# Kernel optimization log

Hardware: AMD Instinct MI355X
Metric: run time of the kernel (lower is better)

## Reference

```python
import jax, jax.numpy as jnp
import numpy as np

N = 50000   # nodes
E = 800000  # edges
F = 64      # num_node_features
H = 64      # hidden_channels
NB = 3      # num_blocks
G = 64      # graphs in batch
C = 10      # num_classes
EPS = 1e-5  # BatchNorm eps


def setup_inputs() -> dict:
    key = jax.random.key(0)
    ks = jax.random.split(key, 24)
    x = jax.random.normal(ks[0], (N, F), dtype=jnp.float32)
    edge_index = jax.random.randint(ks[1], (2, E), 0, N, dtype=jnp.int64)
    batch = jnp.sort(jax.random.randint(ks[2], (N,), 0, G, dtype=jnp.int64))
    s = 0.05
    inp = {
        "x": x, "edge_index": edge_index, "batch": batch,
        "pre_w": jax.random.normal(ks[3], (F, H)) * s,
        "pre_b": jnp.zeros((H,), jnp.float32),
        # stacked per-block params (blocks are structurally identical)
        "blk_prelu1": jnp.full((NB,), 0.25, jnp.float32),
        "blk_bn_gamma": jnp.ones((NB, H), jnp.float32),
        "blk_bn_beta": jnp.zeros((NB, H), jnp.float32),
        "blk_w1": jax.random.normal(ks[4], (NB, H, 2 * H)) * s,
        "blk_b1": jnp.zeros((NB, 2 * H), jnp.float32),
        "blk_prelu2": jnp.full((NB,), 0.25, jnp.float32),
        "blk_w2": jax.random.normal(ks[5], (NB, 2 * H, H)) * s,
        "blk_b2": jnp.zeros((NB, H), jnp.float32),
        "post_bn_gamma": jnp.ones((H,), jnp.float32),
        "post_bn_beta": jnp.zeros((H,), jnp.float32),
        "fc1_w": jax.random.normal(ks[6], (H, 4 * H)) * s,
        "fc1_b": jnp.zeros((4 * H,), jnp.float32),
        "post_prelu": jnp.asarray(0.25, jnp.float32),
        "fc2_w": jax.random.normal(ks[7], (4 * H, C)) * s,
        "fc2_b": jnp.zeros((C,), jnp.float32),
    }
    return inp


def _prelu(x, a):
    return jnp.where(x >= 0, x, a * x)


def _batchnorm(x, gamma, beta):
    # training-mode BN over the node dimension (biased variance), as in torch
    mean = jnp.mean(x, axis=0)
    var = jnp.var(x, axis=0)
    return (x - mean) * jax.lax.rsqrt(var + EPS) * gamma + beta


def _gcn_conv(x, W, bias, src, dst):
    # PyG GCNConv: linear transform, then D^-1/2 (A+I) D^-1/2 aggregation, then bias.
    h = x @ W                                   # [N, out]
    deg = jax.ops.segment_sum(jnp.ones((E,), h.dtype), dst, num_segments=N) + 1.0
    dinv = jax.lax.rsqrt(deg)                   # [N]
    norm = dinv[src] * dinv[dst]                # [E]
    agg = jax.ops.segment_sum(h[src] * norm[:, None], dst, num_segments=N)
    agg = agg + h * (dinv * dinv)[:, None]      # self-loop contribution
    return agg + bias


def reference(x, edge_index, batch, pre_w, pre_b,
              blk_prelu1, blk_bn_gamma, blk_bn_beta, blk_w1, blk_b1,
              blk_prelu2, blk_w2, blk_b2,
              post_bn_gamma, post_bn_beta, fc1_w, fc1_b, post_prelu, fc2_w, fc2_b):
    src, dst = edge_index[0], edge_index[1]
    h = x @ pre_w + pre_b                       # [N, H]
    for i in range(NB):
        h = _prelu(h, blk_prelu1[i])
        h = _batchnorm(h, blk_bn_gamma[i], blk_bn_beta[i])
        h = _gcn_conv(h, blk_w1[i], blk_b1[i], src, dst)   # [N, 2H]
        h = _prelu(h, blk_prelu2[i])
        h = _gcn_conv(h, blk_w2[i], blk_b2[i], src, dst)   # [N, H]
    # global mean pool per graph
    sums = jax.ops.segment_sum(h, batch, num_segments=G)   # [G, H]
    cnts = jax.ops.segment_sum(jnp.ones((N,), h.dtype), batch, num_segments=G)
    pooled = sums / jnp.maximum(cnts, 1.0)[:, None]
    out = _batchnorm(pooled, post_bn_gamma, post_bn_beta)
    out = out @ fc1_w + fc1_b
    out = _prelu(out, post_prelu)
    # dropout with p=0.0 is identity
    out = out @ fc2_w + fc2_b                   # [G, C]
    return out
```

## Files before the change

kernel.cpp:

```cpp
#include <hip/hip_runtime.h>
#include <hip/hip_fp16.h>

#define NN 50000
#define NE 800000
#define NG 64
#define NC 10
#define BN_EPS 1e-5f
#define NSB 196

typedef __attribute__((ext_vector_type(2))) _Float16 h2v;
typedef __attribute__((ext_vector_type(8))) _Float16 f16x8;
typedef __attribute__((ext_vector_type(4))) float f32x4;

__device__ __forceinline__ float2 up2(unsigned u) {
    __half2 h = *reinterpret_cast<__half2*>(&u);
    return __half22float2(h);
}
__device__ __forceinline__ unsigned pk2(float a, float b) {
    __half2 h = __floats2half2_rn(a, b);
    return *reinterpret_cast<unsigned*>(&h);
}
__device__ __forceinline__ float fdot2u(unsigned a, unsigned b, float c) {
    return __builtin_amdgcn_fdot2(__builtin_bit_cast(h2v, a), __builtin_bit_cast(h2v, b), c, false);
}


__global__ void deg_count_kernel(const int* __restrict__ dst, int* __restrict__ deg,
                                 unsigned short* __restrict__ pos16) {
    int e = blockIdx.x * blockDim.x + threadIdx.x;
    if (e < NE) {
        int d = __builtin_nontemporal_load(&dst[e]);
        unsigned short p = (unsigned short)atomicAdd(&deg[d], 1);
        __builtin_nontemporal_store(p, &pos16[e]);
    }
}

__global__ __launch_bounds__(256) void block_sum_kernel(const int* __restrict__ deg,
                                                        int* __restrict__ bsum) {
    int b = blockIdx.x, t = threadIdx.x;
    int n = b * 256 + t;
    int v = (n < NN) ? deg[n] : 0;
    __shared__ int red[256];
    red[t] = v;
    __syncthreads();
    for (int off = 128; off > 0; off >>= 1) {
        if (t < off) red[t] += red[t + off];
        __syncthreads();
    }
    if (t == 0) bsum[b] = red[0];
}

__global__ __launch_bounds__(256) void bsum_scan_kernel(const int* __restrict__ bsum,
                                                        int* __restrict__ boff) {
    __shared__ int s[256];
    int t = threadIdx.x;
    int v = (t < NSB) ? bsum[t] : 0;
    s[t] = v;
    __syncthreads();
    for (int off = 1; off < 256; off <<= 1) {
        int cur = s[t];
        int add = (t >= off) ? s[t - off] : 0;
        __syncthreads();
        s[t] = cur + add;
        __syncthreads();
    }
    if (t < NSB) boff[t] = s[t] - v;
}

__global__ __launch_bounds__(256) void csr_setup_kernel(const int* __restrict__ deg,
                                                        const int* __restrict__ boff,
                                                        int* __restrict__ row_off,
                                                        float* __restrict__ dinv,
                                                        float* __restrict__ rdeg) {
    int b = blockIdx.x, t = threadIdx.x;
    int n = b * 256 + t;
    int v = (n < NN) ? deg[n] : 0;
    __shared__ int s[256];
    s[t] = v;
    __syncthreads();
    for (int off = 1; off < 256; off <<= 1) {
        int cur = s[t];
        int add = (t >= off) ? s[t - off] : 0;
        __syncthreads();
        s[t] = cur + add;
        __syncthreads();
    }
    int excl = s[t] - v + boff[b];
    if (n < NN) {
        row_off[n] = excl;
        float d = (float)v + 1.0f;
        dinv[n] = rsqrtf(d);
        rdeg[n] = sqrtf(d);
    }
    if (n == NN - 1) row_off[NN] = NE;
}

__global__ void scatter_csr_kernel(const int* __restrict__ src, const int* __restrict__ dst,
                                   const unsigned short* __restrict__ pos16,
                                   const int* __restrict__ row_off,
                                   int* __restrict__ csr_src) {
    int e = blockIdx.x * blockDim.x + threadIdx.x;
    if (e >= NE) return;
    int s = __builtin_nontemporal_load(&src[e]);
    int d = __builtin_nontemporal_load(&dst[e]);
    int p = (int)__builtin_nontemporal_load(&pos16[e]);
    csr_src[row_off[d] + p] = s;
}

__global__ void arow_kernel(const int* __restrict__ row_off, const int* __restrict__ csr_src,
                            const float* __restrict__ dinv, float* __restrict__ arow) {
    int n = blockIdx.x * 256 + threadIdx.x;
    if (n >= NN) return;
    float dv = dinv[n];
    float s = dv;
    int e0 = row_off[n], e1 = row_off[n + 1];
    for (int i = e0; i < e1; ++i) s += dinv[csr_src[i]];
    arow[n] = dv * s;
}


__global__ __launch_bounds__(256) void bn_stats_kernel(const __half* __restrict__ h,
                                                       const float* __restrict__ rdeg,
                                                       const float* __restrict__ alpha_p,
                                                       float* __restrict__ stats) {
    float alpha = alpha_p[0];
    int tid = threadIdx.x;
    int c4 = (tid & 15) * 4;
    int rg = tid >> 4;
    float sx = 0, sy = 0, sz = 0, sw = 0;
    float qx = 0, qy = 0, qz = 0, qw = 0;
    for (int n = blockIdx.x * 16 + rg; n < NN; n += gridDim.x * 16) {
        float rd = rdeg[n];
        uint2 u = *(const uint2*)&h[(size_t)n * 64 + c4];
        float2 lo = up2(u.x), hi = up2(u.y);
        float a = lo.x >= 0.f ? lo.x : alpha * lo.x;
        float b = lo.y >= 0.f ? lo.y : alpha * lo.y;
        float c = hi.x >= 0.f ? hi.x : alpha * hi.x;
        float d = hi.y >= 0.f ? hi.y : alpha * hi.y;
        a *= rd; b *= rd; c *= rd; d *= rd;
        sx += a; sy += b; sz += c; sw += d;
        qx += a * a; qy += b * b; qz += c * c; qw += d * d;
    }
    __shared__ float ls[256 * 8];
    float* p = &ls[tid * 8];
    p[0] = sx; p[1] = sy; p[2] = sz; p[3] = sw;
    p[4] = qx; p[5] = qy; p[6] = qz; p[7] = qw;
    __syncthreads();
    if (tid < 128) {
        int cidx = tid >> 3;
        int j = tid & 7;
        float acc = 0.f;
        for (int r = 0; r < 16; ++r) acc += ls[(r * 16 + cidx) * 8 + j];
        int ch = cidx * 4 + (j & 3);
        if (j < 4) atomicAdd(&stats[ch], acc);
        else       atomicAdd(&stats[64 + ch], acc);
    }
}


template <bool PRELU, int OUT>
__global__ __launch_bounds__(256) void gather_kernel(const int* __restrict__ row_off,
                                                     const int* __restrict__ csr_src,
                                                     const float* __restrict__ dinv,
                                                     const float* __restrict__ bias,
                                                     const float* __restrict__ alpha_p,
                                                     const __half* __restrict__ hh,
                                                     __half* __restrict__ outp) {
    int tid = threadIdx.x;
    int r = blockIdx.x * 32 + (tid >> 3);
    int c = blockIdx.y * 32 + (tid & 7) * 4;
    if (r >= NN) return;
    float alpha = 0.f;
    if constexpr (PRELU) alpha = alpha_p[0];
    uint2 u0 = *(const uint2*)&hh[(size_t)r * 64 + c];
    float2 slo = up2(u0.x), shi = up2(u0.y);
    float ax = slo.x, ay = slo.y, az = shi.x, aw = shi.y;
    if constexpr (PRELU) {
        ax = ax >= 0.f ? ax : alpha * ax;
        ay = ay >= 0.f ? ay : alpha * ay;
        az = az >= 0.f ? az : alpha * az;
        aw = aw >= 0.f ? aw : alpha * aw;
    }
    int beg = row_off[r];
    int end = row_off[r + 1];
    int i = beg;
    for (; i + 3 < end; i += 4) {
        int s0 = csr_src[i], s1 = csr_src[i + 1], s2 = csr_src[i + 2], s3 = csr_src[i + 3];
        uint2 v0 = *(const uint2*)&hh[(size_t)s0 * 64 + c];
        uint2 v1 = *(const uint2*)&hh[(size_t)s1 * 64 + c];
        uint2 v2 = *(const uint2*)&hh[(size_t)s2 * 64 + c];
        uint2 v3 = *(const uint2*)&hh[(size_t)s3 * 64 + c];
        float2 a0 = up2(v0.x), b0 = up2(v0.y);
        float2 a1 = up2(v1.x), b1 = up2(v1.y);
        float2 a2 = up2(v2.x), b2 = up2(v2.y);
        float2 a3 = up2(v3.x), b3 = up2(v3.y);
        if constexpr (PRELU) {
            a0.x = a0.x >= 0.f ? a0.x : alpha * a0.x;  a0.y = a0.y >= 0.f ? a0.y : alpha * a0.y;
            b0.x = b0.x >= 0.f ? b0.x : alpha * b0.x;  b0.y = b0.y >= 0.f ? b0.y : alpha * b0.y;
            a1.x = a1.x >= 0.f ? a1.x : alpha * a1.x;  a1.y = a1.y >= 0.f ? a1.y : alpha * a1.y;
            b1.x = b1.x >= 0.f ? b1.x : alpha * b1.x;  b1.y = b1.y >= 0.f ? b1.y : alpha * b1.y;
            a2.x = a2.x >= 0.f ? a2.x : alpha * a2.x;  a2.y = a2.y >= 0.f ? a2.y : alpha * a2.y;
            b2.x = b2.x >= 0.f ? b2.x : alpha * b2.x;  b2.y = b2.y >= 0.f ? b2.y : alpha * b2.y;
            a3.x = a3.x >= 0.f ? a3.x : alpha * a3.x;  a3.y = a3.y >= 0.f ? a3.y : alpha * a3.y;
            b3.x = b3.x >= 0.f ? b3.x : alpha * b3.x;  b3.y = b3.y >= 0.f ? b3.y : alpha * b3.y;
        }
        ax += (a0.x + a1.x) + (a2.x + a3.x);
        ay += (a0.y + a1.y) + (a2.y + a3.y);
        az += (b0.x + b1.x) + (b2.x + b3.x);
        aw += (b0.y + b1.y) + (b2.y + b3.y);
    }
    for (; i < end; ++i) {
        int s0 = csr_src[i];
        uint2 v0 = *(const uint2*)&hh[(size_t)s0 * 64 + c];
        float2 a0 = up2(v0.x), b0 = up2(v0.y);
        if constexpr (PRELU) {
            a0.x = a0.x >= 0.f ? a0.x : alpha * a0.x;  a0.y = a0.y >= 0.f ? a0.y : alpha * a0.y;
            b0.x = b0.x >= 0.f ? b0.x : alpha * b0.x;  b0.y = b0.y >= 0.f ? b0.y : alpha * b0.y;
        }
        ax += a0.x; ay += a0.y; az += b0.x; aw += b0.y;
    }
    float dv = dinv[r];
    float ox, oy, oz, ow;
    if constexpr (OUT == 2) {
        ox = dv * ax; oy = dv * ay; oz = dv * az; ow = dv * aw;
    } else {
        float4 b = *(const float4*)&bias[c];
        ox = dv * ax + b.x; oy = dv * ay + b.y; oz = dv * az + b.z; ow = dv * aw + b.w;
        if constexpr (OUT == 1) {
            ox *= dv; oy *= dv; oz *= dv; ow *= dv;
        }
    }
    uint2 o;
    o.x = pk2(ox, oy);
    o.y = pk2(oz, ow);
    *(uint2*)&outp[(size_t)r * 64 + c] = o;
}


__global__ __launch_bounds__(256) void gemm_pre_kernel(const float* __restrict__ Af,
                                                       const float* __restrict__ W,
                                                       __half* __restrict__ outp,
                                                       const float* __restrict__ bias,
                                                       const float* __restrict__ dinv) {
    constexpr int K = 64, M = 64, BM = 128;
    constexpr int CG = M / 8;
    constexpr int RG = 256 / CG;
    constexpr int KP = K / 2;
    __shared__ unsigned Wh[KP * M];
    __shared__ unsigned Ahs[BM][KP + 4];
    int tid = threadIdx.x;
    for (int i = tid; i < KP * M; i += 256) {
        int kp = i / M, j = i % M;
        Wh[i] = pk2(W[(2 * kp) * M + j], W[(2 * kp + 1) * M + j]);
    }
    int r0 = blockIdx.x * BM;
    for (int i = tid; i < BM * (K / 4); i += 256) {
        int row = i / (K / 4);
        int k4 = (i % (K / 4)) * 4;
        int rr = r0 + row;
        if (rr > NN - 1) rr = NN - 1;
        float4 v = *(const float4*)&Af[(size_t)rr * K + k4];
        uint2 o;
        o.x = pk2(v.x, v.y);
        o.y = pk2(v.z, v.w);
        *(uint2*)&Ahs[row][k4 >> 1] = o;
    }
    __syncthreads();
    int cg = tid % CG, rg = tid / CG;
    int c = cg * 8;
    float acc[4][8];
#pragma unroll
    for (int r = 0; r < 4; ++r)
#pragma unroll
        for (int j = 0; j < 8; ++j) acc[r][j] = 0.f;
#pragma unroll 4
    for (int kp = 0; kp < KP; kp += 2) {
        uint2 a2[4];
#pragma unroll
        for (int r = 0; r < 4; ++r) a2[r] = *(const uint2*)&Ahs[rg + r * RG][kp];
#pragma unroll
        for (int kk = 0; kk < 2; ++kk) {
            const unsigned* wp = &Wh[(kp + kk) * M + c];
            uint4 w0 = *(const uint4*)wp;
            uint4 w1 = *(const uint4*)(wp + 4);
#pragma unroll
            for (int r = 0; r < 4; ++r) {
                unsigned av = kk ? a2[r].y : a2[r].x;
                acc[r][0] = fdot2u(av, w0.x, acc[r][0]);
                acc[r][1] = fdot2u(av, w0.y, acc[r][1]);
                acc[r][2] = fdot2u(av, w0.z, acc[r][2]);
                acc[r][3] = fdot2u(av, w0.w, acc[r][3]);
                acc[r][4] = fdot2u(av, w1.x, acc[r][4]);
                acc[r][5] = fdot2u(av, w1.y, acc[r][5]);
                acc[r][6] = fdot2u(av, w1.z, acc[r][6]);
                acc[r][7] = fdot2u(av, w1.w, acc[r][7]);
            }
        }
    }
    float4 b0 = *(const float4*)&bias[c];
    float4 b1 = *(const float4*)&bias[c + 4];
#pragma unroll
    for (int r = 0; r < 4; ++r) {
        int row = r0 + rg + r * RG;
        if (row < NN) {
            float sc = dinv[row];
            uint4 o;
            o.x = pk2((acc[r][0] + b0.x) * sc, (acc[r][1] + b0.y) * sc);
            o.y = pk2((acc[r][2] + b0.z) * sc, (acc[r][3] + b0.w) * sc);
            o.z = pk2((acc[r][4] + b1.x) * sc, (acc[r][5] + b1.y) * sc);
            o.w = pk2((acc[r][6] + b1.z) * sc, (acc[r][7] + b1.w) * sc);
            *(uint4*)&outp[(size_t)row * M + c] = o;
        }
    }
}


__global__ __launch_bounds__(256) void mfma_gemm1_kernel(const __half* __restrict__ t,
                                                         const float* __restrict__ W1,
                                                         const float* __restrict__ b1,
                                                         __half* __restrict__ u,
                                                         const float* __restrict__ stats,
                                                         const float* __restrict__ gamma,
                                                         const float* __restrict__ beta,
                                                         const float* __restrict__ arow) {
    __shared__ _Float16 At[128][72];
    __shared__ _Float16 Wt[128][72];
    __shared__ float scS[64], shS[64];
    int tid = threadIdx.x;
    if (tid < 64) {
        float mean = stats[tid] * (1.0f / NN);
        float var  = stats[64 + tid] * (1.0f / NN) - mean * mean;
        float sc = gamma[tid] * rsqrtf(var + BN_EPS);
        scS[tid] = sc;
        shS[tid] = beta[tid] - mean * sc;
    }
    for (int i = tid; i < 128 * 32; i += 256) {
        int j = i & 127;
        int k2 = i >> 7;
        *(unsigned*)&Wt[j][2 * k2] = pk2(W1[(2 * k2) * 128 + j], W1[(2 * k2 + 1) * 128 + j]);
    }
    __syncthreads();
    int r0 = blockIdx.x * 128;
    for (int i = tid; i < 128 * 16; i += 256) {
        int row = i >> 4;
        int k4 = (i & 15) * 4;
        int rr = r0 + row;
        if (rr > NN - 1) rr = NN - 1;
        uint2 uu = *(const uint2*)&t[(size_t)rr * 64 + k4];
        float2 lo = up2(uu.x), hi = up2(uu.y);
        float av = arow[rr];
        float vx = lo.x * scS[k4 + 0] + shS[k4 + 0] * av;
        float vy = lo.y * scS[k4 + 1] + shS[k4 + 1] * av;
        float vz = hi.x * scS[k4 + 2] + shS[k4 + 2] * av;
        float vw = hi.y * scS[k4 + 3] + shS[k4 + 3] * av;
        *(unsigned*)&At[row][k4]     = pk2(vx, vy);
        *(unsigned*)&At[row][k4 + 2] = pk2(vz, vw);
    }
    __syncthreads();
    int w = tid >> 6;
    int l = tid & 63;
    int lr = l & 15;
    int lk = (l >> 4) * 8;
    f32x4 acc[2][8];
#pragma unroll
    for (int rt = 0; rt < 2; ++rt)
#pragma unroll
        for (int ct = 0; ct < 8; ++ct) acc[rt][ct] = (f32x4){0.f, 0.f, 0.f, 0.f};
#pragma unroll
    for (int k0 = 0; k0 < 64; k0 += 32) {
        f16x8 a0 = *(const f16x8*)&At[w * 32 + lr][k0 + lk];
        f16x8 a1 = *(const f16x8*)&At[w * 32 + 16 + lr][k0 + lk];
#pragma unroll
        for (int ct = 0; ct < 8; ++ct) {
            f16x8 b = *(const f16x8*)&Wt[ct * 16 + lr][k0 + lk];
            acc[0][ct] = __builtin_amdgcn_mfma_f32_16x16x32_f16(a0, b, acc[0][ct], 0, 0, 0);
            acc[1][ct] = __builtin_amdgcn_mfma_f32_16x16x32_f16(a1, b, acc[1][ct], 0, 0, 0);
        }
    }
    int rowbase = r0 + w * 32 + (l >> 4) * 4;
#pragma unroll
    for (int rt = 0; rt < 2; ++rt) {
#pragma unroll
        for (int ct = 0; ct < 8; ++ct) {
            int col = ct * 16 + lr;
            float bb = b1[col];
#pragma unroll
            for (int r = 0; r < 4; ++r) {
                int row = rowbase + rt * 16 + r;
                if (row < NN) u[(size_t)row * 128 + col] = __float2half(acc[rt][ct][r] + bb);
            }
        }
    }
}


__global__ __launch_bounds__(256) void mfma_gemm2_kernel(const __half* __restrict__ u,
                                                         const float* __restrict__ W2,
                                                         const float* __restrict__ alpha_p,
                                                         const float* __restrict__ dinv,
                                                         __half* __restrict__ t) {
    __shared__ _Float16 Ut[64][136];
    __shared__ _Float16 Wt[64][136];
    int tid = threadIdx.x;
    float alpha = alpha_p[0];
    for (int i = tid; i < 64 * 64; i += 256) {
        int j = i & 63;
        int k2 = i >> 6;
        *(unsigned*)&Wt[j][2 * k2] = pk2(W2[(2 * k2) * 64 + j], W2[(2 * k2 + 1) * 64 + j]);
    }
    int r0 = blockIdx.x * 64;
    for (int i = tid; i < 64 * 32; i += 256) {
        int row = i >> 5;
        int k4 = (i & 31) * 4;
        int rr = r0 + row;
        if (rr > NN - 1) rr = NN - 1;
        uint2 uu = *(const uint2*)&u[(size_t)rr * 128 + k4];
        float2 lo = up2(uu.x), hi = up2(uu.y);
        float vx = lo.x >= 0.f ? lo.x : alpha * lo.x;
        float vy = lo.y >= 0.f ? lo.y : alpha * lo.y;
        float vz = hi.x >= 0.f ? hi.x : alpha * hi.x;
        float vw = hi.y >= 0.f ? hi.y : alpha * hi.y;
        *(unsigned*)&Ut[row][k4]     = pk2(vx, vy);
        *(unsigned*)&Ut[row][k4 + 2] = pk2(vz, vw);
    }
    __syncthreads();
    int w = tid >> 6;
    int l = tid & 63;
    int lr = l & 15;
    int lk = (l >> 4) * 8;
    f32x4 acc[4];
#pragma unroll
    for (int ct = 0; ct < 4; ++ct) acc[ct] = (f32x4){0.f, 0.f, 0.f, 0.f};
#pragma unroll
    for (int k0 = 0; k0 < 128; k0 += 32) {
        f16x8 a = *(const f16x8*)&Ut[w * 16 + lr][k0 + lk];
#pragma unroll
        for (int ct = 0; ct < 4; ++ct) {
            f16x8 b = *(const f16x8*)&Wt[ct * 16 + lr][k0 + lk];
            acc[ct] = __builtin_amdgcn_mfma_f32_16x16x32_f16(a, b, acc[ct], 0, 0, 0);
        }
    }
    int rowbase = r0 + w * 16 + (l >> 4) * 4;
#pragma unroll
    for (int ct = 0; ct < 4; ++ct) {
        int col = ct * 16 + lr;
#pragma unroll
        for (int r = 0; r < 4; ++r) {
            int row = rowbase + r;
            if (row < NN) t[(size_t)row * 64 + col] = __float2half(acc[ct][r] * dinv[row]);
        }
    }
}


__global__ __launch_bounds__(256) void pool_seg_kernel(const __half* __restrict__ h,
                                                       const int* __restrict__ batch,
                                                       float* __restrict__ pooled) {
    int g = blockIdx.x;
    __shared__ int sbeg, send;
    int tid = threadIdx.x;
    if (tid == 0) {
        int lo = 0, hi = NN;
        while (lo < hi) { int mid = (lo + hi) >> 1; if (batch[mid] < g) lo = mid + 1; else hi = mid; }
        sbeg = lo;
        lo = 0; hi = NN;
        while (lo < hi) { int mid = (lo + hi) >> 1; if (batch[mid] < g + 1) lo = mid + 1; else hi = mid; }
        send = lo;
    }
    __syncthreads();
    int beg = sbeg, end = send;
    int c4 = (tid & 15) * 4;
    int rg = tid >> 4;
    float sx = 0, sy = 0, sz = 0, sw = 0;
    for (int n = beg + rg; n < end; n += 16) {
        uint2 u = *(const uint2*)&h[(size_t)n * 64 + c4];
        float2 lo = up2(u.x), hi = up2(u.y);
        sx += lo.x; sy += lo.y; sz += hi.x; sw += hi.y;
    }
    __shared__ float red[256 * 4];
    float* p = &red[tid * 4];
    p[0] = sx; p[1] = sy; p[2] = sz; p[3] = sw;
    __syncthreads();
    if (tid < 64) {
        int cg = tid >> 2;
        int j = tid & 3;
        float acc = 0.f;
        for (int r = 0; r < 16; ++r) acc += red[(r * 16 + cg) * 4 + j];
        float cnt = fmaxf((float)(end - beg), 1.0f);
        pooled[g * 64 + cg * 4 + j] = acc / cnt;
    }
}


__global__ __launch_bounds__(64) void head_stats_kernel(const float* __restrict__ pooled,
                                                        const float* __restrict__ gamma,
                                                        const float* __restrict__ beta,
                                                        float* __restrict__ headsc) {
    int ch = threadIdx.x;
    float s = 0.f, q = 0.f;
    for (int g = 0; g < 64; ++g) {
        float v = pooled[g * 64 + ch];
        s += v; q += v * v;
    }
    float mean = s * (1.0f / 64.0f);
    float var = q * (1.0f / 64.0f) - mean * mean;
    float sc = gamma[ch] * rsqrtf(var + BN_EPS);
    headsc[ch] = sc;
    headsc[64 + ch] = beta[ch] - mean * sc;
}

__global__ __launch_bounds__(256) void head_fc_kernel(const float* __restrict__ pooled,
                                                      const float* __restrict__ headsc,
                                                      const float* __restrict__ fc1w,
                                                      const float* __restrict__ fc1b,
                                                      const float* __restrict__ prelu_p,
                                                      const float* __restrict__ fc2w,
                                                      const float* __restrict__ fc2b,
                                                      float* __restrict__ out) {
    int g = blockIdx.x;
    int tid = threadIdx.x;
    __shared__ float pr[64];
    __shared__ float red[256];
    if (tid < 64) pr[tid] = pooled[g * 64 + tid] * headsc[tid] + headsc[64 + tid];
    __syncthreads();
    float alpha = prelu_p[0];
    float o1 = fc1b[tid];
    for (int k = 0; k < 64; ++k) o1 += pr[k] * fc1w[k * 256 + tid];
    o1 = o1 >= 0.f ? o1 : alpha * o1;
    for (int c = 0; c < NC; ++c) {
        red[tid] = o1 * fc2w[tid * NC + c];
        __syncthreads();
        for (int off = 128; off > 0; off >>= 1) {
            if (tid < off) red[tid] += red[tid + off];
            __syncthreads();
        }
        if (tid == 0) out[g * NC + c] = red[0] + fc2b[c];
        __syncthreads();
    }
}


extern "C" void kernel_launch(void* const* d_in, const int* in_sizes, int n_in,
                              void* d_out, int out_size, void* d_ws, size_t ws_size,
                              hipStream_t stream) {
    const float* x       = (const float*)d_in[0];
    const int*   ei      = (const int*)d_in[1];
    const int*   batch   = (const int*)d_in[2];
    const float* pre_w   = (const float*)d_in[3];
    const float* pre_b   = (const float*)d_in[4];
    const float* bp1     = (const float*)d_in[5];
    const float* bng     = (const float*)d_in[6];
    const float* bnb     = (const float*)d_in[7];
    const float* bw1     = (const float*)d_in[8];
    const float* bb1     = (const float*)d_in[9];
    const float* bp2     = (const float*)d_in[10];
    const float* bw2     = (const float*)d_in[11];
    const float* bb2     = (const float*)d_in[12];
    const float* pgamma  = (const float*)d_in[13];
    const float* pbeta   = (const float*)d_in[14];
    const float* fc1w    = (const float*)d_in[15];
    const float* fc1b    = (const float*)d_in[16];
    const float* pprelu  = (const float*)d_in[17];
    const float* fc2w    = (const float*)d_in[18];
    const float* fc2b    = (const float*)d_in[19];

    const int* src = ei;
    const int* dst = ei + NE;

    __half* hA16 = (__half*)d_ws;
    __half* t16  = hA16 + (size_t)NN * 64;
    __half* u16  = t16 + (size_t)NN * 64;
    float* dinv  = (float*)(u16 + (size_t)NN * 128);
    float* rdeg  = dinv + NN;
    float* arow  = rdeg + NN;
    float* stats = arow + NN;
    float* pooledg = stats + 3 * 128;
    float* headsc  = pooledg + 64 * 64;
    int*   csr_src = (int*)(headsc + 128);
    int*   row_off = csr_src + NE;
    int*   deg     = row_off + NN + 1;
    int*   bsum    = deg + NN;
    int*   boff    = bsum + NSB;
    unsigned short* pos16 = (unsigned short*)(boff + NSB);

    hipMemsetAsync(stats, 0, (size_t)3 * 128 * 4, stream);
    hipMemsetAsync(deg, 0, (size_t)NN * 4, stream);

    deg_count_kernel<<<(NE + 255) / 256, 256, 0, stream>>>(dst, deg, pos16);
    block_sum_kernel<<<NSB, 256, 0, stream>>>(deg, bsum);
    bsum_scan_kernel<<<1, 256, 0, stream>>>(bsum, boff);
    csr_setup_kernel<<<NSB, 256, 0, stream>>>(deg, boff, row_off, dinv, rdeg);
    scatter_csr_kernel<<<(NE + 255) / 256, 256, 0, stream>>>(src, dst, pos16, row_off, csr_src);
    arow_kernel<<<(NN + 255) / 256, 256, 0, stream>>>(row_off, csr_src, dinv, arow);

    gemm_pre_kernel<<<(NN + 127) / 128, 256, 0, stream>>>(x, pre_w, hA16, pre_b, dinv);

    dim3 ggrid((NN + 31) / 32, 2);
    for (int i = 0; i < 3; ++i) {
        const float* a1 = bp1 + i;
        const float* a2 = bp2 + i;
        const float* gm = bng + i * 64;
        const float* bt = bnb + i * 64;
        const float* w1 = bw1 + (size_t)i * 64 * 128;
        const float* b1 = bb1 + i * 128;
        const float* w2 = bw2 + (size_t)i * 128 * 64;
        const float* b2 = bb2 + i * 64;
        float* st = stats + i * 128;

        bn_stats_kernel<<<256, 256, 0, stream>>>(hA16, rdeg, a1, st);
        gather_kernel<true, 2><<<ggrid, 256, 0, stream>>>(
            row_off, csr_src, dinv, nullptr, a1, hA16, t16);
        mfma_gemm1_kernel<<<(NN + 127) / 128, 256, 0, stream>>>(
            t16, w1, b1, u16, st, gm, bt, arow);
        mfma_gemm2_kernel<<<(NN + 63) / 64, 256, 0, stream>>>(
            u16, w2, a2, dinv, t16);
        if (i < 2) {
            gather_kernel<false, 1><<<ggrid, 256, 0, stream>>>(
                row_off, csr_src, dinv, b2, nullptr, t16, hA16);
        } else {
            gather_kernel<false, 0><<<ggrid, 256, 0, stream>>>(
                row_off, csr_src, dinv, b2, nullptr, t16, hA16);
        }
    }

    pool_seg_kernel<<<NG, 256, 0, stream>>>(hA16, batch, pooledg);
    head_stats_kernel<<<1, 64, 0, stream>>>(pooledg, pgamma, pbeta, headsc);
    head_fc_kernel<<<NG, 256, 0, stream>>>(pooledg, headsc, fc1w, fc1b, pprelu,
                                           fc2w, fc2b, (float*)d_out);
}
```

Baseline: 402.5 us.

## Fuse BN stats into gather, merge the two MLP GEMMs, partition CSR scatter

Per-channel BatchNorm statistics are now computed inside the first gather kernel from the self-row load, which removes the separate stats pass. The two MFMA GEMMs are fused into one kernel that keeps the 128-wide intermediate (with PReLU applied) in shared memory instead of writing and re-reading it from global memory. The CSR scatter is split into four passes by destination range, meant to improve write locality at the cost of reading the edge list four times. The fused GEMM uses 64-row tiles and a larger shared footprint, which may lower occupancy.

```diff
diff --git a/kernel.cpp b/kernel.cpp
--- a/kernel.cpp
+++ b/kernel.cpp
@@ -95,14 +95,15 @@
     if (n == NN - 1) row_off[NN] = NE;
 }
 
-__global__ void scatter_csr_kernel(const int* __restrict__ src, const int* __restrict__ dst,
-                                   const unsigned short* __restrict__ pos16,
-                                   const int* __restrict__ row_off,
-                                   int* __restrict__ csr_src) {
+__global__ void scatter_pass_kernel(const int* __restrict__ src, const int* __restrict__ dst,
+                                    const unsigned short* __restrict__ pos16,
+                                    const int* __restrict__ row_off,
+                                    int* __restrict__ csr_src, int d0, int d1) {
     int e = blockIdx.x * blockDim.x + threadIdx.x;
     if (e >= NE) return;
+    int d = __builtin_nontemporal_load(&dst[e]);
+    if (d < d0 || d >= d1) return;
     int s = __builtin_nontemporal_load(&src[e]);
-    int d = __builtin_nontemporal_load(&dst[e]);
     int p = (int)__builtin_nontemporal_load(&pos16[e]);
     csr_src[row_off[d] + p] = s;
 }
@@ -119,77 +120,63 @@
 }
 
 
-__global__ __launch_bounds__(256) void bn_stats_kernel(const __half* __restrict__ h,
-                                                       const float* __restrict__ rdeg,
-                                                       const float* __restrict__ alpha_p,
-                                                       float* __restrict__ stats) {
-    float alpha = alpha_p[0];
-    int tid = threadIdx.x;
-    int c4 = (tid & 15) * 4;
-    int rg = tid >> 4;
-    float sx = 0, sy = 0, sz = 0, sw = 0;
-    float qx = 0, qy = 0, qz = 0, qw = 0;
-    for (int n = blockIdx.x * 16 + rg; n < NN; n += gridDim.x * 16) {
-        float rd = rdeg[n];
-        uint2 u = *(const uint2*)&h[(size_t)n * 64 + c4];
-        float2 lo = up2(u.x), hi = up2(u.y);
-        float a = lo.x >= 0.f ? lo.x : alpha * lo.x;
-        float b = lo.y >= 0.f ? lo.y : alpha * lo.y;
-        float c = hi.x >= 0.f ? hi.x : alpha * hi.x;
-        float d = hi.y >= 0.f ? hi.y : alpha * hi.y;
-        a *= rd; b *= rd; c *= rd; d *= rd;
-        sx += a; sy += b; sz += c; sw += d;
-        qx += a * a; qy += b * b; qz += c * c; qw += d * d;
-    }
-    __shared__ float ls[256 * 8];
-    float* p = &ls[tid * 8];
-    p[0] = sx; p[1] = sy; p[2] = sz; p[3] = sw;
-    p[4] = qx; p[5] = qy; p[6] = qz; p[7] = qw;
-    __syncthreads();
-    if (tid < 128) {
-        int cidx = tid >> 3;
-        int j = tid & 7;
-        float acc = 0.f;
-        for (int r = 0; r < 16; ++r) acc += ls[(r * 16 + cidx) * 8 + j];
-        int ch = cidx * 4 + (j & 3);
-        if (j < 4) atomicAdd(&stats[ch], acc);
-        else       atomicAdd(&stats[64 + ch], acc);
-    }
-}
-
-
-template <bool PRELU, int OUT>
+template <bool PRELU, int OUT, bool STATS>
 __global__ __launch_bounds__(256) void gather_kernel(const int* __restrict__ row_off,
                                                      const int* __restrict__ csr_src,
                                                      const float* __restrict__ dinv,
+                                                     const float* __restrict__ rdeg,
                                                      const float* __restrict__ bias,
                                                      const float* __restrict__ alpha_p,
                                                      const __half* __restrict__ hh,
-                                                     __half* __restrict__ outp) {
+                                                     __half* __restrict__ outp,
+                                                     float* __restrict__ stats) {
     int tid = threadIdx.x;
     int r = blockIdx.x * 32 + (tid >> 3);
     int c = blockIdx.y * 32 + (tid & 7) * 4;
-    if (r >= NN) return;
+    bool valid = r < NN;
+    if constexpr (!STATS) {
+        if (!valid) return;
+    }
+    int rc = valid ? r : NN - 1;
     float alpha = 0.f;
     if constexpr (PRELU) alpha = alpha_p[0];
-    uint2 u0 = *(const uint2*)&hh[(size_t)r * 64 + c];
+    uint2 u0 = *(const uint2*)&hh[(size_t)rc * 64 + c];
     float2 slo = up2(u0.x), shi = up2(u0.y);
-    float ax = slo.x, ay = slo.y, az = shi.x, aw = shi.y;
+    float s0 = slo.x, s1 = slo.y, s2 = shi.x, s3 = shi.y;
     if constexpr (PRELU) {
-        ax = ax >= 0.f ? ax : alpha * ax;
-        ay = ay >= 0.f ? ay : alpha * ay;
-        az = az >= 0.f ? az : alpha * az;
-        aw = aw >= 0.f ? aw : alpha * aw;
-    }
+        s0 = s0 >= 0.f ? s0 : alpha * s0;
+        s1 = s1 >= 0.f ? s1 : alpha * s1;
+        s2 = s2 >= 0.f ? s2 : alpha * s2;
+        s3 = s3 >= 0.f ? s3 : alpha * s3;
+    }
+    if constexpr (STATS) {
+        __shared__ float st[256][8];
+        float rd = valid ? rdeg[rc] : 0.f;
+        float m0 = s0 * rd, m1 = s1 * rd, m2 = s2 * rd, m3 = s3 * rd;
+        float* p = st[tid];
+        p[0] = m0; p[1] = m1; p[2] = m2; p[3] = m3;
+        p[4] = m0 * m0; p[5] = m1 * m1; p[6] = m2 * m2; p[7] = m3 * m3;
+        __syncthreads();
+        if (tid < 64) {
+            int lane8 = tid & 7;
+            int j = tid >> 3;
+            float acc = 0.f;
+            for (int row = 0; row < 32; ++row) acc += st[row * 8 + lane8][j];
+            int ch = blockIdx.y * 32 + lane8 * 4 + (j & 3);
+            atomicAdd(&stats[(j < 4 ? 0 : 64) + ch], acc);
+        }
+        if (!valid) return;
+    }
+    float ax = s0, ay = s1, az = s2, aw = s3;
     int beg = row_off[r];
     int end = row_off[r + 1];
     int i = beg;
     for (; i + 3 < end; i += 4) {
-        int s0 = csr_src[i], s1 = csr_src[i + 1], s2 = csr_src[i + 2], s3 = csr_src[i + 3];
-        uint2 v0 = *(const uint2*)&hh[(size_t)s0 * 64 + c];
-        uint2 v1 = *(const uint2*)&hh[(size_t)s1 * 64 + c];
-        uint2 v2 = *(const uint2*)&hh[(size_t)s2 * 64 + c];
-        uint2 v3 = *(const uint2*)&hh[(size_t)s3 * 64 + c];
+        int q0 = csr_src[i], q1 = csr_src[i + 1], q2 = csr_src[i + 2], q3 = csr_src[i + 3];
+        uint2 v0 = *(const uint2*)&hh[(size_t)q0 * 64 + c];
+        uint2 v1 = *(const uint2*)&hh[(size_t)q1 * 64 + c];
+        uint2 v2 = *(const uint2*)&hh[(size_t)q2 * 64 + c];
+        uint2 v3 = *(const uint2*)&hh[(size_t)q3 * 64 + c];
         float2 a0 = up2(v0.x), b0 = up2(v0.y);
         float2 a1 = up2(v1.x), b1 = up2(v1.y);
         float2 a2 = up2(v2.x), b2 = up2(v2.y);
@@ -210,8 +197,8 @@
         aw += (b0.y + b1.y) + (b2.y + b3.y);
     }
     for (; i < end; ++i) {
-        int s0 = csr_src[i];
-        uint2 v0 = *(const uint2*)&hh[(size_t)s0 * 64 + c];
+        int q0 = csr_src[i];
+        uint2 v0 = *(const uint2*)&hh[(size_t)q0 * 64 + c];
         float2 a0 = up2(v0.x), b0 = up2(v0.y);
         if constexpr (PRELU) {
             a0.x = a0.x >= 0.f ? a0.x : alpha * a0.x;  a0.y = a0.y >= 0.f ? a0.y : alpha * a0.y;
@@ -315,16 +302,21 @@
 }
 
 
-__global__ __launch_bounds__(256) void mfma_gemm1_kernel(const __half* __restrict__ t,
-                                                         const float* __restrict__ W1,
-                                                         const float* __restrict__ b1,
-                                                         __half* __restrict__ u,
-                                                         const float* __restrict__ stats,
-                                                         const float* __restrict__ gamma,
-                                                         const float* __restrict__ beta,
-                                                         const float* __restrict__ arow) {
-    __shared__ _Float16 At[128][72];
-    __shared__ _Float16 Wt[128][72];
+__global__ __launch_bounds__(256) void mfma_mlp_kernel(__half* __restrict__ t,
+                                                       const float* __restrict__ W1,
+                                                       const float* __restrict__ b1,
+                                                       const float* __restrict__ W2,
+                                                       const float* __restrict__ alpha2_p,
+                                                       const float* __restrict__ stats,
+                                                       const float* __restrict__ gamma,
+                                                       const float* __restrict__ beta,
+                                                       const float* __restrict__ arow,
+                                                       const float* __restrict__ dinv) {
+    __shared__ __align__(16) char smem[45056];
+    auto Wt1 = (_Float16(*)[72])smem;
+    auto Wt2 = (_Float16(*)[136])smem;
+    auto At  = (_Float16(*)[72])(smem + 18432);
+    auto Ut  = (_Float16(*)[136])(smem + 27648);
     __shared__ float scS[64], shS[64];
     int tid = threadIdx.x;
     if (tid < 64) {
@@ -337,11 +329,10 @@
     for (int i = tid; i < 128 * 32; i += 256) {
         int j = i & 127;
         int k2 = i >> 7;
-        *(unsigned*)&Wt[j][2 * k2] = pk2(W1[(2 * k2) * 128 + j], W1[(2 * k2 + 1) * 128 + j]);
-    }
-    __syncthreads();
-    int r0 = blockIdx.x * 128;
-    for (int i = tid; i < 128 * 16; i += 256) {
+        *(unsigned*)&Wt1[j][2 * k2] = pk2(W1[(2 * k2) * 128 + j], W1[(2 * k2 + 1) * 128 + j]);
+    }
+    int r0 = blockIdx.x * 64;
+    for (int i = tid; i < 64 * 16; i += 256) {
         int row = i >> 4;
         int k4 = (i & 15) * 4;
         int rr = r0 + row;
@@ -361,93 +352,61 @@
     int l = tid & 63;
     int lr = l & 15;
     int lk = (l >> 4) * 8;
-    f32x4 acc[2][8];
-#pragma unroll
-    for (int rt = 0; rt < 2; ++rt)
-#pragma unroll
-        for (int ct = 0; ct < 8; ++ct) acc[rt][ct] = (f32x4){0.f, 0.f, 0.f, 0.f};
-#pragma unroll
-    for (int k0 = 0; k0 < 64; k0 += 32) {
-        f16x8 a0 = *(const f16x8*)&At[w * 32 + lr][k0 + lk];
-        f16x8 a1 = *(const f16x8*)&At[w * 32 + 16 + lr][k0 + lk];
-#pragma unroll
-        for (int ct = 0; ct < 8; ++ct) {
-            f16x8 b = *(const f16x8*)&Wt[ct * 16 + lr][k0 + lk];
-            acc[0][ct] = __builtin_amdgcn_mfma_f32_16x16x32_f16(a0, b, acc[0][ct], 0, 0, 0);
-            acc[1][ct] = __builtin_amdgcn_mfma_f32_16x16x32_f16(a1, b, acc[1][ct], 0, 0, 0);
-        }
-    }
-    int rowbase = r0 + w * 32 + (l >> 4) * 4;
-#pragma unroll
-    for (int rt = 0; rt < 2; ++rt) {
+    int rloc = w * 16 + (l >> 4) * 4;
+    {
+        f32x4 acc[8];
+#pragma unroll
+        for (int ct = 0; ct < 8; ++ct) acc[ct] = (f32x4){0.f, 0.f, 0.f, 0.f};
+#pragma unroll
+        for (int k0 = 0; k0 < 64; k0 += 32) {
+            f16x8 a = *(const f16x8*)&At[w * 16 + lr][k0 + lk];
+#pragma unroll
+            for (int ct = 0; ct < 8; ++ct) {
+                f16x8 b = *(const f16x8*)&Wt1[ct * 16 + lr][k0 + lk];
+                acc[ct] = __builtin_amdgcn_mfma_f32_16x16x32_f16(a, b, acc[ct], 0, 0, 0);
+            }
+        }
+        float alpha = alpha2_p[0];
 #pragma unroll
         for (int ct = 0; ct < 8; ++ct) {
             int col = ct * 16 + lr;
             float bb = b1[col];
 #pragma unroll
             for (int r = 0; r < 4; ++r) {
-                int row = rowbase + rt * 16 + r;
-                if (row < NN) u[(size_t)row * 128 + col] = __float2half(acc[rt][ct][r] + bb);
+                float v = acc[ct][r] + bb;
+                v = v >= 0.f ? v : alpha * v;
+                Ut[rloc + r][col] = (_Float16)v;
             }
         }
     }
-}
-
-
-__global__ __launch_bounds__(256) void mfma_gemm2_kernel(const __half* __restrict__ u,
-                                                         const float* __restrict__ W2,
-                                                         const float* __restrict__ alpha_p,
-                                                         const float* __restrict__ dinv,
-                                                         __half* __restrict__ t) {
-    __shared__ _Float16 Ut[64][136];
-    __shared__ _Float16 Wt[64][136];
-    int tid = threadIdx.x;
-    float alpha = alpha_p[0];
+    __syncthreads();
     for (int i = tid; i < 64 * 64; i += 256) {
         int j = i & 63;
         int k2 = i >> 6;
-        *(unsigned*)&Wt[j][2 * k2] = pk2(W2[(2 * k2) * 64 + j], W2[(2 * k2 + 1) * 64 + j]);
-    }
-    int r0 = blockIdx.x * 64;
-    for (int i = tid; i < 64 * 32; i += 256) {
-        int row = i >> 5;
-        int k4 = (i & 31) * 4;
-        int rr = r0 + row;
-        if (rr > NN - 1) rr = NN - 1;
-        uint2 uu = *(const uint2*)&u[(size_t)rr * 128 + k4];
-        float2 lo = up2(uu.x), hi = up2(uu.y);
-        float vx = lo.x >= 0.f ? lo.x : alpha * lo.x;
-        float vy = lo.y >= 0.f ? lo.y : alpha * lo.y;
-        float vz = hi.x >= 0.f ? hi.x : alpha * hi.x;
-        float vw = hi.y >= 0.f ? hi.y : alpha * hi.y;
-        *(unsigned*)&Ut[row][k4]     = pk2(vx, vy);
-        *(unsigned*)&Ut[row][k4 + 2] = pk2(vz, vw);
-    }
-    __syncthreads();
-    int w = tid >> 6;
-    int l = tid & 63;
-    int lr = l & 15;
-    int lk = (l >> 4) * 8;
-    f32x4 acc[4];
-#pragma unroll
-    for (int ct = 0; ct < 4; ++ct) acc[ct] = (f32x4){0.f, 0.f, 0.f, 0.f};
-#pragma unroll
-    for (int k0 = 0; k0 < 128; k0 += 32) {
-        f16x8 a = *(const f16x8*)&Ut[w * 16 + lr][k0 + lk];
+        *(unsigned*)&Wt2[j][2 * k2] = pk2(W2[(2 * k2) * 64 + j], W2[(2 * k2 + 1) * 64 + j]);
+    }
+    __syncthreads();
+    {
+        f32x4 acc[4];
+#pragma unroll
+        for (int ct = 0; ct < 4; ++ct) acc[ct] = (f32x4){0.f, 0.f, 0.f, 0.f};
+#pragma unroll
+        for (int k0 = 0; k0 < 128; k0 += 32) {
+            f16x8 a = *(const f16x8*)&Ut[w * 16 + lr][k0 + lk];
+#pragma unroll
+            for (int ct = 0; ct < 4; ++ct) {
+                f16x8 b = *(const f16x8*)&Wt2[ct * 16 + lr][k0 + lk];
+                acc[ct] = __builtin_amdgcn_mfma_f32_16x16x32_f16(a, b, acc[ct], 0, 0, 0);
+            }
+        }
 #pragma unroll
         for (int ct = 0; ct < 4; ++ct) {
-            f16x8 b = *(const f16x8*)&Wt[ct * 16 + lr][k0 + lk];
-            acc[ct] = __builtin_amdgcn_mfma_f32_16x16x32_f16(a, b, acc[ct], 0, 0, 0);
-        }
-    }
-    int rowbase = r0 + w * 16 + (l >> 4) * 4;
-#pragma unroll
-    for (int ct = 0; ct < 4; ++ct) {
-        int col = ct * 16 + lr;
-#pragma unroll
-        for (int r = 0; r < 4; ++r) {
-            int row = rowbase + r;
-            if (row < NN) t[(size_t)row * 64 + col] = __float2half(acc[ct][r] * dinv[row]);
+            int col = ct * 16 + lr;
+#pragma unroll
+            for (int r = 0; r < 4; ++r) {
+                int row = r0 + rloc + r;
+                if (row < NN) t[(size_t)row * 64 + col] = __float2half(acc[ct][r] * dinv[row]);
+            }
         }
     }
 }
@@ -569,8 +528,7 @@
 
     __half* hA16 = (__half*)d_ws;
     __half* t16  = hA16 + (size_t)NN * 64;
-    __half* u16  = t16 + (size_t)NN * 64;
-    float* dinv  = (float*)(u16 + (size_t)NN * 128);
+    float* dinv  = (float*)(t16 + (size_t)NN * 64);
     float* rdeg  = dinv + NN;
     float* arow  = rdeg + NN;
     float* stats = arow + NN;
@@ -590,7 +548,12 @@
     block_sum_kernel<<<NSB, 256, 0, stream>>>(deg, bsum);
     bsum_scan_kernel<<<1, 256, 0, stream>>>(bsum, boff);
     csr_setup_kernel<<<NSB, 256, 0, stream>>>(deg, boff, row_off, dinv, rdeg);
-    scatter_csr_kernel<<<(NE + 255) / 256, 256, 0, stream>>>(src, dst, pos16, row_off, csr_src);
+    for (int p = 0; p < 4; ++p) {
+        int d0 = p * 12500;
+        int d1 = (p == 3) ? NN : d0 + 12500;
+        scatter_pass_kernel<<<(NE + 255) / 256, 256, 0, stream>>>(
+            src, dst, pos16, row_off, csr_src, d0, d1);
+    }
     arow_kernel<<<(NN + 255) / 256, 256, 0, stream>>>(row_off, csr_src, dinv, arow);
 
     gemm_pre_kernel<<<(NN + 127) / 128, 256, 0, stream>>>(x, pre_w, hA16, pre_b, dinv);
@@ -607,19 +570,16 @@
         const float* b2 = bb2 + i * 64;
         float* st = stats + i * 128;
 
-        bn_stats_kernel<<<256, 256, 0, stream>>>(hA16, rdeg, a1, st);
-        gather_kernel<true, 2><<<ggrid, 256, 0, stream>>>(
-            row_off, csr_src, dinv, nullptr, a1, hA16, t16);
-        mfma_gemm1_kernel<<<(NN + 127) / 128, 256, 0, stream>>>(
-            t16, w1, b1, u16, st, gm, bt, arow);
-        mfma_gemm2_kernel<<<(NN + 63) / 64, 256, 0, stream>>>(
-            u16, w2, a2, dinv, t16);
+        gather_kernel<true, 2, true><<<ggrid, 256, 0, stream>>>(
+            row_off, csr_src, dinv, rdeg, nullptr, a1, hA16, t16, st);
+        mfma_mlp_kernel<<<(NN + 63) / 64, 256, 0, stream>>>(
+            t16, w1, b1, w2, a2, st, gm, bt, arow, dinv);
         if (i < 2) {
-            gather_kernel<false, 1><<<ggrid, 256, 0, stream>>>(
-                row_off, csr_src, dinv, b2, nullptr, t16, hA16);
+            gather_kernel<false, 1, false><<<ggrid, 256, 0, stream>>>(
+                row_off, csr_src, dinv, rdeg, b2, nullptr, t16, hA16, nullptr);
         } else {
-            gather_kernel<false, 0><<<ggrid, 256, 0, stream>>>(
-                row_off, csr_src, dinv, b2, nullptr, t16, hA16);
+            gather_kernel<false, 0, false><<<ggrid, 256, 0, stream>>>(
+                row_off, csr_src, dinv, rdeg, b2, nullptr, t16, hA16, nullptr);
         }
     }
 
```

Result: slower. 446.3 us (+10.9%).
